# Performance work log

Hardware: AMD Instinct MI355X
Metric: run time of the kernel (lower is better)

The kernel has to match this reference:

```python
import jax, jax.numpy as jnp
import numpy as np

NEG_SLOPE = 0.05

def leaky(x):
    return jnp.where(x >= 0, x, NEG_SLOPE * x)

def segment_softmax(e, seg, num_segments):
    m = jax.ops.segment_max(e, seg, num_segments=num_segments)
    ex = jnp.exp(e - m[seg])
    s = jax.ops.segment_sum(ex, seg, num_segments=num_segments)
    return ex / s[seg]

def scatter_mean(vals, seg, num_segments):
    tot = jax.ops.segment_sum(vals, seg, num_segments=num_segments)
    cnt = jax.ops.segment_sum(jnp.ones((vals.shape[0],), vals.dtype), seg, num_segments=num_segments)
    return tot / jnp.maximum(cnt, 1.0)[:, None]

def setup_inputs() -> dict:
    key = jax.random.key(0)
    ks = jax.random.split(key, 7)
    N, E, Fn, Fe, D = 50000, 800000, 128, 64, 64
    return {
        "x": jax.random.normal(ks[0], (N, Fn), jnp.float32),
        "edge_attr": jax.random.normal(ks[1], (E, Fe), jnp.float32),
        "edge_index": jax.random.randint(ks[2], (2, E), 0, N, jnp.int64),
        "W_node": jax.random.normal(ks[3], (D, Fn), jnp.float32) * 0.05,
        "W_edge": jax.random.normal(ks[4], (D, Fe), jnp.float32) * 0.05,
        "a_node": jax.random.normal(ks[5], (2 * D,), jnp.float32) * 0.05,
        "a_edge": jax.random.normal(ks[6], (2 * D,), jnp.float32) * 0.05,
    }

def reference(x, edge_attr, edge_index, W_node, W_edge, a_node, a_edge):
    N = x.shape[0]
    E = edge_index.shape[1]
    D = W_node.shape[0]
    h = x @ W_node.T           # [N, D]
    g = edge_attr @ W_edge.T   # [E, D]

    # ----- node->node branch (with self loops) -----
    loops = jnp.arange(N, dtype=edge_index.dtype)
    i_idx = jnp.concatenate([edge_index[0], loops])  # targets [E+N]
    j_idx = jnp.concatenate([edge_index[1], loops])  # sources [E+N]
    # attention score a^T [h_i || h_j] split into halves (no concat materialized)
    hi = h @ a_node[:D]   # [N]
    hj = h @ a_node[D:]   # [N]
    e_n = leaky(hi[i_idx] + hj[j_idx])               # [E+N]
    alpha_n = segment_softmax(e_n, i_idx, N)
    x_from_nodes = scatter_mean(alpha_n[:, None] * h[j_idx], i_idx, N)  # [N, D]

    # ----- edge->node branch (each edge attends from both endpoints) -----
    i_idx_e = jnp.concatenate([edge_index[0], edge_index[1]])           # [2E]
    g2 = jnp.concatenate([g, g], axis=0)                                # g[k_idx_e], [2E, D]
    he = h @ a_edge[:D]   # [N]
    ge = g @ a_edge[D:]   # [E]
    ge2 = jnp.concatenate([ge, ge])
    e_e = leaky(he[i_idx_e] + ge2)                                      # [2E]
    alpha_e = segment_softmax(e_e, i_idx_e, N)
    x_from_edges = scatter_mean(alpha_e[:, None] * g2, i_idx_e, N)      # [N, D]

    return jnp.concatenate([leaky(x_from_nodes), leaky(x_from_edges)], axis=-1)  # [N, 2D]
```

## Files before the change

kernel.cpp:

```cpp
#include <hip/hip_runtime.h>
#include <math.h>

#define NEG_SLOPE 0.05f

__device__ __forceinline__ float leaky(float x){ return x >= 0.f ? x : NEG_SLOPE * x; }

__device__ __forceinline__ unsigned short f2bf(float f){
    unsigned u = __float_as_uint(f);
    unsigned r = u + 0x7FFFu + ((u >> 16) & 1u);
    return (unsigned short)(r >> 16);
}
__device__ __forceinline__ float bf2f(unsigned short us){
    return __uint_as_float((unsigned)us << 16);
}

__global__ __launch_bounds__(256) void k_init(int* deg_n, int* deg_o, int* ctr,
        float* __restrict__ vv, const float* __restrict__ We, const float* __restrict__ a_edge, int N){
    int t = blockIdx.x * blockDim.x + threadIdx.x;
    if (t == 0){ ctr[0] = 0; ctr[1] = 0; }
    if (t < 64){
        float s = 0.f;
        for (int d = 0; d < 64; d++) s = fmaf(We[d * 64 + t], a_edge[64 + d], s);
        vv[t] = s;
    }
    int stride = gridDim.x * blockDim.x;
    for (int i = t; i < N; i += stride){ deg_n[i] = 0; deg_o[i] = 0; }
}

__global__ __launch_bounds__(256) void k_gemm_h(const float* __restrict__ A, const float* __restrict__ B,
        const float* __restrict__ a_node, const float* __restrict__ a_edge,
        float* __restrict__ C, unsigned short* __restrict__ Cb,
        float* __restrict__ hi, float* __restrict__ hj, float* __restrict__ he, int M){
    const int K = 128;
    __shared__ float As[K][68];
    __shared__ float Bs[K][68];
    const int m0 = blockIdx.x * 64;
    const int t = threadIdx.x;
    for (int i = t; i < 16 * K; i += 256){
        int d = i & 63, kq = i >> 6;
        float4 b = *(const float4*)&B[(size_t)d * K + kq * 4];
        Bs[kq*4+0][d] = b.x; Bs[kq*4+1][d] = b.y; Bs[kq*4+2][d] = b.z; Bs[kq*4+3][d] = b.w;
    }
    for (int i = t; i < 16 * K; i += 256){
        int r = i & 63, kq = i >> 6;
        int m = m0 + r;
        float4 a = make_float4(0.f, 0.f, 0.f, 0.f);
        if (m < M) a = *(const float4*)&A[(size_t)m * K + kq * 4];
        As[kq*4+0][r] = a.x; As[kq*4+1][r] = a.y; As[kq*4+2][r] = a.z; As[kq*4+3][r] = a.w;
    }
    __syncthreads();
    const int tx = t & 15, ty = t >> 4;
    float acc[4][4] = {};
    #pragma unroll 4
    for (int k = 0; k < K; k++){
        float4 a4 = *(const float4*)&As[k][ty * 4];
        float4 b4 = *(const float4*)&Bs[k][tx * 4];
        float av[4] = {a4.x, a4.y, a4.z, a4.w};
        float bv[4] = {b4.x, b4.y, b4.z, b4.w};
        #pragma unroll
        for (int r = 0; r < 4; r++)
            #pragma unroll
            for (int c = 0; c < 4; c++)
                acc[r][c] = fmaf(av[r], bv[c], acc[r][c]);
    }
    #pragma unroll
    for (int r = 0; r < 4; r++){
        int m = m0 + ty * 4 + r;
        if (m < M){
            float4 o = make_float4(acc[r][0], acc[r][1], acc[r][2], acc[r][3]);
            *(float4*)&C[(size_t)m * 64 + tx * 4] = o;
            uint2 u;
            u.x = (unsigned)f2bf(o.x) | ((unsigned)f2bf(o.y) << 16);
            u.y = (unsigned)f2bf(o.z) | ((unsigned)f2bf(o.w) << 16);
            *(uint2*)&Cb[(size_t)m * 64 + tx * 4] = u;
        }
    }
    float4 an1 = *(const float4*)&a_node[tx * 4];
    float4 an2 = *(const float4*)&a_node[64 + tx * 4];
    float4 ae1 = *(const float4*)&a_edge[tx * 4];
    float p1[4], p2[4], p3[4];
    #pragma unroll
    for (int r = 0; r < 4; r++){
        p1[r] = acc[r][0]*an1.x + acc[r][1]*an1.y + acc[r][2]*an1.z + acc[r][3]*an1.w;
        p2[r] = acc[r][0]*an2.x + acc[r][1]*an2.y + acc[r][2]*an2.z + acc[r][3]*an2.w;
        p3[r] = acc[r][0]*ae1.x + acc[r][1]*ae1.y + acc[r][2]*ae1.z + acc[r][3]*ae1.w;
    }
    #pragma unroll
    for (int m = 1; m < 16; m <<= 1){
        #pragma unroll
        for (int r = 0; r < 4; r++){
            p1[r] += __shfl_xor(p1[r], m);
            p2[r] += __shfl_xor(p2[r], m);
            p3[r] += __shfl_xor(p3[r], m);
        }
    }
    if (tx == 0){
        #pragma unroll
        for (int r = 0; r < 4; r++){
            int m = m0 + ty * 4 + r;
            if (m < M){ hi[m] = p1[r]; hj[m] = p2[r]; he[m] = p3[r]; }
        }
    }
}

__global__ __launch_bounds__(256) void k_ge2(const float* __restrict__ ea, const int* __restrict__ idx,
        const float* __restrict__ vv, float* __restrict__ ge, unsigned short* __restrict__ eab,
        int* __restrict__ deg_n, int* __restrict__ deg_o, int E){
    int l = threadIdx.x & 63;
    int gw = (blockIdx.x * 256 + threadIdx.x) >> 6;
    int nw = (gridDim.x * 256) >> 6;
    int seg = l & 15, rl = l >> 4;
    float4 v4 = *(const float4*)&vv[seg * 4];
    for (int r0 = gw * 4; r0 < E; r0 += nw * 4){
        int row = r0 + rl;
        if (row < E){
            float4 a = *(const float4*)&ea[(size_t)row * 64 + seg * 4];
            float s = a.x*v4.x + a.y*v4.y + a.z*v4.z + a.w*v4.w;
            uint2 u;
            u.x = (unsigned)f2bf(a.x) | ((unsigned)f2bf(a.y) << 16);
            u.y = (unsigned)f2bf(a.z) | ((unsigned)f2bf(a.w) << 16);
            *(uint2*)&eab[(size_t)row * 64 + seg * 4] = u;
            #pragma unroll
            for (int m = 1; m < 16; m <<= 1) s += __shfl_xor(s, m);
            if (seg == 0){
                ge[row] = s;
                int i0 = idx[row], i1 = idx[E + row];
                atomicAdd(&deg_n[i0], 1);
                atomicAdd(&deg_o[i1], 1);
            }
        }
    }
}

__global__ __launch_bounds__(256) void k_off(const int* __restrict__ deg_n, const int* __restrict__ deg_o,
        int* __restrict__ deg_e,
        int* __restrict__ off_n, int* __restrict__ cur_n,
        int* __restrict__ off_e, int* __restrict__ cur_e,
        int* __restrict__ ctr, int N){
    int i = blockIdx.x * 256 + threadIdx.x;
    int lane = threadIdx.x & 63;
    int dn = 0, de = 0;
    if (i < N){
        dn = deg_n[i];
        de = dn + deg_o[i];
    }
    int pn = dn, pe = de;
    #pragma unroll
    for (int d = 1; d < 64; d <<= 1){
        int on = __shfl_up(pn, d), oe = __shfl_up(pe, d);
        if (lane >= d){ pn += on; pe += oe; }
    }
    int base_n = 0, base_e = 0;
    if (lane == 63){
        base_n = atomicAdd(&ctr[0], pn);
        base_e = atomicAdd(&ctr[1], pe);
    }
    base_n = __shfl(base_n, 63);
    base_e = __shfl(base_e, 63);
    if (i < N){
        int on = base_n + pn - dn;
        int oe = base_e + pe - de;
        off_n[i] = on; cur_n[i] = on;
        off_e[i] = oe; cur_e[i] = oe;
        deg_e[i] = de;
    }
}

__global__ __launch_bounds__(256) void k_fill(const int* __restrict__ idx,
        const float* __restrict__ hj, const float* __restrict__ ge,
        int* __restrict__ cur_n, int* __restrict__ cur_e,
        int2* __restrict__ adj_n, int2* __restrict__ adj_e, int E, int N){
    int g = blockIdx.x & 7;
    int lo = (int)(((long long)g * N) >> 3), hi = (int)(((long long)(g + 1) * N) >> 3);
    int nblk = gridDim.x >> 3;
    int start = ((blockIdx.x >> 3) * 256) + threadIdx.x;
    int stride = nblk * 256;
    for (int k = start; k < E; k += stride){
        int i0 = idx[k], i1 = idx[E + k];
        bool t0 = (i0 >= lo && i0 < hi), t1 = (i1 >= lo && i1 < hi);
        if (t0 | t1){
            int gb = __float_as_int(ge[k]);
            if (t0){
                adj_n[atomicAdd(&cur_n[i0], 1)] = make_int2(i1, __float_as_int(hj[i1]));
                adj_e[atomicAdd(&cur_e[i0], 1)] = make_int2(k, gb);
            }
            if (t1) adj_e[atomicAdd(&cur_e[i1], 1)] = make_int2(k, gb);
        }
    }
}

__global__ __launch_bounds__(256) void k_out(const float* __restrict__ h,
        const unsigned short* __restrict__ hb, const unsigned short* __restrict__ eab,
        const float* __restrict__ hi, const float* __restrict__ hj, const float* __restrict__ he,
        const float* __restrict__ We,
        const int* __restrict__ off_n, const int* __restrict__ deg_n, const int2* __restrict__ adj_n,
        const int* __restrict__ off_e, const int* __restrict__ deg_e, const int2* __restrict__ adj_e,
        float* __restrict__ out, int N, int nb_node){
    __shared__ float WeT[64][65];
    __shared__ float valS[4][64];
    int lane = threadIdx.x & 63;
    int w = threadIdx.x >> 6;

    if (blockIdx.x < nb_node){
        int i = (blockIdx.x * 256 + (int)threadIdx.x) >> 6;
        if (i >= N) return;
        float hi_i = hi[i];
        float wself = __expf(leaky(hi_i + hj[i]));
        float s = wself;
        float acc = wself * h[(size_t)i * 64 + lane];
        int cnt = deg_n[i];
        int p = off_n[i], e = p + cnt;
        for (; p + 4 <= e; p += 4){
            int2 r0 = adj_n[p], r1 = adj_n[p+1], r2 = adj_n[p+2], r3 = adj_n[p+3];
            float v0 = bf2f(hb[(size_t)r0.x * 64 + lane]);
            float v1 = bf2f(hb[(size_t)r1.x * 64 + lane]);
            float v2 = bf2f(hb[(size_t)r2.x * 64 + lane]);
            float v3 = bf2f(hb[(size_t)r3.x * 64 + lane]);
            float w0 = __expf(leaky(hi_i + __int_as_float(r0.y)));
            float w1 = __expf(leaky(hi_i + __int_as_float(r1.y)));
            float w2 = __expf(leaky(hi_i + __int_as_float(r2.y)));
            float w3 = __expf(leaky(hi_i + __int_as_float(r3.y)));
            acc = fmaf(w0, v0, acc); acc = fmaf(w1, v1, acc);
            acc = fmaf(w2, v2, acc); acc = fmaf(w3, v3, acc);
            s += (w0 + w1) + (w2 + w3);
        }
        for (; p < e; p++){
            int2 r = adj_n[p];
            float v = bf2f(hb[(size_t)r.x * 64 + lane]);
            float wgt = __expf(leaky(hi_i + __int_as_float(r.y)));
            acc = fmaf(wgt, v, acc); s += wgt;
        }
        out[(size_t)i * 128 + lane] = leaky(acc / s / (float)(cnt + 1));
    } else {
        for (int t2 = threadIdx.x; t2 < 1024; t2 += 256){
            int d = t2 >> 4, c0 = (t2 & 15) * 4;
            float4 v = *(const float4*)&We[d * 64 + c0];
            WeT[c0+0][d] = v.x; WeT[c0+1][d] = v.y; WeT[c0+2][d] = v.z; WeT[c0+3][d] = v.w;
        }
        int i = ((blockIdx.x - nb_node) * 256 + (int)threadIdx.x) >> 6;
        float val = 0.f;
        int iok = (i < N);
        if (iok){
            float he_i = he[i];
            float s = 0.f, acc = 0.f;
            int cnt = deg_e[i];
            int p = off_e[i], e = p + cnt;
            for (; p + 4 <= e; p += 4){
                int2 r0 = adj_e[p], r1 = adj_e[p+1], r2 = adj_e[p+2], r3 = adj_e[p+3];
                float v0 = bf2f(eab[(size_t)r0.x * 64 + lane]);
                float v1 = bf2f(eab[(size_t)r1.x * 64 + lane]);
                float v2 = bf2f(eab[(size_t)r2.x * 64 + lane]);
                float v3 = bf2f(eab[(size_t)r3.x * 64 + lane]);
                float w0 = __expf(leaky(he_i + __int_as_float(r0.y)));
                float w1 = __expf(leaky(he_i + __int_as_float(r1.y)));
                float w2 = __expf(leaky(he_i + __int_as_float(r2.y)));
                float w3 = __expf(leaky(he_i + __int_as_float(r3.y)));
                acc = fmaf(w0, v0, acc); acc = fmaf(w1, v1, acc);
                acc = fmaf(w2, v2, acc); acc = fmaf(w3, v3, acc);
                s += (w0 + w1) + (w2 + w3);
            }
            for (; p < e; p++){
                int2 r = adj_e[p];
                float v = bf2f(eab[(size_t)r.x * 64 + lane]);
                float wgt = __expf(leaky(he_i + __int_as_float(r.y)));
                acc = fmaf(wgt, v, acc); s += wgt;
            }
            val = (cnt > 0) ? (acc / s / (float)cnt) : 0.f;
        }
        __syncthreads();
        valS[w][lane] = val;
        __syncthreads();
        if (iok){
            float acc2 = 0.f;
            #pragma unroll
            for (int c4 = 0; c4 < 16; c4++){
                float4 vb = *(const float4*)&valS[w][c4 * 4];
                acc2 = fmaf(vb.x, WeT[c4*4+0][lane], acc2);
                acc2 = fmaf(vb.y, WeT[c4*4+1][lane], acc2);
                acc2 = fmaf(vb.z, WeT[c4*4+2][lane], acc2);
                acc2 = fmaf(vb.w, WeT[c4*4+3][lane], acc2);
            }
            out[(size_t)i * 128 + 64 + lane] = leaky(acc2);
        }
    }
}

extern "C" void kernel_launch(void* const* d_in, const int* in_sizes, int n_in,
                              void* d_out, int out_size, void* d_ws, size_t ws_size,
                              hipStream_t stream){
    const float* x      = (const float*)d_in[0];
    const float* ea     = (const float*)d_in[1];
    const int*   idx    = (const int*)  d_in[2];
    const float* Wn     = (const float*)d_in[3];
    const float* We     = (const float*)d_in[4];
    const float* a_node = (const float*)d_in[5];
    const float* a_edge = (const float*)d_in[6];
    float* out = (float*)d_out;

    const int N = in_sizes[0] / 128;
    const int E = in_sizes[1] / 64;

    float* p = (float*)d_ws;
    float* h      = p; p += (size_t)N * 64;
    float* hi     = p; p += N;
    float* hj     = p; p += N;
    float* he     = p; p += N;
    float* ge     = p; p += E;
    float* vv     = p; p += 64;
    unsigned short* hb  = (unsigned short*)p; p += (size_t)N * 32;
    unsigned short* eab = (unsigned short*)p; p += (size_t)E * 32;
    int* deg_n = (int*)p; p += N;
    int* deg_o = (int*)p; p += N;
    int* deg_e = (int*)p; p += N;
    int* off_n = (int*)p; p += N;
    int* off_e = (int*)p; p += N;
    int* cur_n = (int*)p; p += N;
    int* cur_e = (int*)p; p += N;
    int* ctr   = (int*)p; p += 4;
    int2* adj_n = (int2*)p; p += (size_t)2 * E;
    int2* adj_e = (int2*)p; p += (size_t)4 * E;

    const int nb = (N + 3) / 4;

    k_init<<<256, 256, 0, stream>>>(deg_n, deg_o, ctr, vv, We, a_edge, N);
    k_gemm_h<<<(N + 63) / 64, 256, 0, stream>>>(x, Wn, a_node, a_edge, h, hb, hi, hj, he, N);
    k_ge2<<<2048, 256, 0, stream>>>(ea, idx, vv, ge, eab, deg_n, deg_o, E);
    k_off<<<(N + 255) / 256, 256, 0, stream>>>(deg_n, deg_o, deg_e, off_n, cur_n, off_e, cur_e, ctr, N);
    k_fill<<<1024, 256, 0, stream>>>(idx, hj, ge, cur_n, cur_e, adj_n, adj_e, E, N);
    k_out<<<2 * nb, 256, 0, stream>>>(h, hb, eab, hi, hj, he, We,
                                      off_n, deg_n, adj_n, off_e, deg_e, adj_e, out, N, nb);
}
```

Before: 611.8 us.

## Vectorize gather rows per quarter-wave and make CSR slices contiguous per fill group

The aggregation kernels now have each 16-lane quarter-wave process a different neighbor, loading 4 bf16 values per lane, so one wave handles 4 neighbors at a time. Partial sums are combined with cross-lane shuffles at the end. The offset computation is split into two passes that compute per-slice totals, so each of the 8 node slices used by the fill kernel gets a contiguous, 64-aligned region of the adjacency arrays. This is meant to improve memory-level parallelism in the gather and locality in the fill scatter, at the cost of an extra kernel launch and more shuffle work.

```diff
diff --git a/kernel.cpp b/kernel.cpp
--- a/kernel.cpp
+++ b/kernel.cpp
@@ -14,10 +14,21 @@
     return __uint_as_float((unsigned)us << 16);
 }
 
-__global__ __launch_bounds__(256) void k_init(int* deg_n, int* deg_o, int* ctr,
+__device__ __forceinline__ int slice_lo(int g, int N){
+    long long v = ((((long long)g * N) >> 3) + 63LL) & ~63LL;
+    return (int)(v > (long long)N ? (long long)N : v);
+}
+__device__ __forceinline__ int slice_of_wave(int w0, int N){
+    int g = 0;
+    #pragma unroll
+    for (int q = 1; q < 8; q++) if (w0 >= slice_lo(q, N)) g = q;
+    return g;
+}
+
+__global__ __launch_bounds__(256) void k_init(int* deg_n, int* deg_o, int* sctr,
         float* __restrict__ vv, const float* __restrict__ We, const float* __restrict__ a_edge, int N){
     int t = blockIdx.x * blockDim.x + threadIdx.x;
-    if (t == 0){ ctr[0] = 0; ctr[1] = 0; }
+    if (t < 32) sctr[t] = 0;
     if (t < 64){
         float s = 0.f;
         for (int d = 0; d < 64; d++) s = fmaf(We[d * 64 + t], a_edge[64 + d], s);
@@ -132,28 +143,48 @@
     }
 }
 
-__global__ __launch_bounds__(256) void k_off(const int* __restrict__ deg_n, const int* __restrict__ deg_o,
+__global__ __launch_bounds__(256) void k_off_a(const int* __restrict__ deg_n, const int* __restrict__ deg_o,
+        int* __restrict__ sctr, int N){
+    int i = blockIdx.x * 256 + threadIdx.x;
+    int lane = threadIdx.x & 63;
+    int dn = 0, de = 0;
+    if (i < N){ dn = deg_n[i]; de = dn + deg_o[i]; }
+    int pn = dn, pe = de;
+    #pragma unroll
+    for (int d = 1; d < 64; d <<= 1){ pn += __shfl_xor(pn, d); pe += __shfl_xor(pe, d); }
+    if (lane == 0){
+        int w0 = i;
+        if (w0 < N){
+            int g = slice_of_wave(w0, N);
+            atomicAdd(&sctr[g], pn);
+            atomicAdd(&sctr[8 + g], pe);
+        }
+    }
+}
+
+__global__ __launch_bounds__(256) void k_off_b(const int* __restrict__ deg_n, const int* __restrict__ deg_o,
         int* __restrict__ deg_e,
         int* __restrict__ off_n, int* __restrict__ cur_n,
         int* __restrict__ off_e, int* __restrict__ cur_e,
-        int* __restrict__ ctr, int N){
+        int* __restrict__ sctr, int N){
     int i = blockIdx.x * 256 + threadIdx.x;
     int lane = threadIdx.x & 63;
     int dn = 0, de = 0;
-    if (i < N){
-        dn = deg_n[i];
-        de = dn + deg_o[i];
-    }
+    if (i < N){ dn = deg_n[i]; de = dn + deg_o[i]; }
     int pn = dn, pe = de;
     #pragma unroll
     for (int d = 1; d < 64; d <<= 1){
         int on = __shfl_up(pn, d), oe = __shfl_up(pe, d);
         if (lane >= d){ pn += on; pe += oe; }
     }
+    int w0 = i - lane;
     int base_n = 0, base_e = 0;
-    if (lane == 63){
-        base_n = atomicAdd(&ctr[0], pn);
-        base_e = atomicAdd(&ctr[1], pe);
+    if (lane == 63 && w0 < N){
+        int g = slice_of_wave(w0, N);
+        int bn = 0, be = 0;
+        for (int q = 0; q < g; q++){ bn += sctr[q]; be += sctr[8 + q]; }
+        base_n = bn + atomicAdd(&sctr[16 + g], pn);
+        base_e = be + atomicAdd(&sctr[24 + g], pe);
     }
     base_n = __shfl(base_n, 63);
     base_e = __shfl(base_e, 63);
@@ -171,7 +202,7 @@
         int* __restrict__ cur_n, int* __restrict__ cur_e,
         int2* __restrict__ adj_n, int2* __restrict__ adj_e, int E, int N){
     int g = blockIdx.x & 7;
-    int lo = (int)(((long long)g * N) >> 3), hi = (int)(((long long)(g + 1) * N) >> 3);
+    int lo = slice_lo(g, N), hi = slice_lo(g + 1, N);
     int nblk = gridDim.x >> 3;
     int start = ((blockIdx.x >> 3) * 256) + threadIdx.x;
     int stride = nblk * 256;
@@ -198,39 +229,74 @@
         float* __restrict__ out, int N, int nb_node){
     __shared__ float WeT[64][65];
     __shared__ float valS[4][64];
-    int lane = threadIdx.x & 63;
-    int w = threadIdx.x >> 6;
+    const int lane = threadIdx.x & 63;
+    const int w = threadIdx.x >> 6;
+    const int rl = lane >> 4, seg = lane & 15;
 
     if (blockIdx.x < nb_node){
         int i = (blockIdx.x * 256 + (int)threadIdx.x) >> 6;
         if (i >= N) return;
         float hi_i = hi[i];
-        float wself = __expf(leaky(hi_i + hj[i]));
-        float s = wself;
-        float acc = wself * h[(size_t)i * 64 + lane];
         int cnt = deg_n[i];
-        int p = off_n[i], e = p + cnt;
-        for (; p + 4 <= e; p += 4){
-            int2 r0 = adj_n[p], r1 = adj_n[p+1], r2 = adj_n[p+2], r3 = adj_n[p+3];
-            float v0 = bf2f(hb[(size_t)r0.x * 64 + lane]);
-            float v1 = bf2f(hb[(size_t)r1.x * 64 + lane]);
-            float v2 = bf2f(hb[(size_t)r2.x * 64 + lane]);
-            float v3 = bf2f(hb[(size_t)r3.x * 64 + lane]);
-            float w0 = __expf(leaky(hi_i + __int_as_float(r0.y)));
-            float w1 = __expf(leaky(hi_i + __int_as_float(r1.y)));
-            float w2 = __expf(leaky(hi_i + __int_as_float(r2.y)));
-            float w3 = __expf(leaky(hi_i + __int_as_float(r3.y)));
-            acc = fmaf(w0, v0, acc); acc = fmaf(w1, v1, acc);
-            acc = fmaf(w2, v2, acc); acc = fmaf(w3, v3, acc);
-            s += (w0 + w1) + (w2 + w3);
-        }
-        for (; p < e; p++){
-            int2 r = adj_n[p];
-            float v = bf2f(hb[(size_t)r.x * 64 + lane]);
-            float wgt = __expf(leaky(hi_i + __int_as_float(r.y)));
-            acc = fmaf(wgt, v, acc); s += wgt;
-        }
-        out[(size_t)i * 128 + lane] = leaky(acc / s / (float)(cnt + 1));
+        int p = off_n[i];
+        int e = p + cnt;
+        float a0 = 0.f, a1 = 0.f, a2 = 0.f, a3 = 0.f, sp = 0.f;
+        for (; p + 8 <= e; p += 8){
+            int2 ra = adj_n[p + rl];
+            int2 rb = adj_n[p + 4 + rl];
+            uint2 ua = *(const uint2*)&hb[(size_t)ra.x * 64 + seg * 4];
+            uint2 ub = *(const uint2*)&hb[(size_t)rb.x * 64 + seg * 4];
+            float wa = __expf(leaky(hi_i + __int_as_float(ra.y)));
+            float wb = __expf(leaky(hi_i + __int_as_float(rb.y)));
+            a0 = fmaf(wa, bf2f((unsigned short)ua.x), a0);
+            a1 = fmaf(wa, bf2f((unsigned short)(ua.x >> 16)), a1);
+            a2 = fmaf(wa, bf2f((unsigned short)ua.y), a2);
+            a3 = fmaf(wa, bf2f((unsigned short)(ua.y >> 16)), a3);
+            a0 = fmaf(wb, bf2f((unsigned short)ub.x), a0);
+            a1 = fmaf(wb, bf2f((unsigned short)(ub.x >> 16)), a1);
+            a2 = fmaf(wb, bf2f((unsigned short)ub.y), a2);
+            a3 = fmaf(wb, bf2f((unsigned short)(ub.y >> 16)), a3);
+            sp += wa + wb;
+        }
+        if (p + 4 <= e){
+            int2 ra = adj_n[p + rl];
+            uint2 ua = *(const uint2*)&hb[(size_t)ra.x * 64 + seg * 4];
+            float wa = __expf(leaky(hi_i + __int_as_float(ra.y)));
+            a0 = fmaf(wa, bf2f((unsigned short)ua.x), a0);
+            a1 = fmaf(wa, bf2f((unsigned short)(ua.x >> 16)), a1);
+            a2 = fmaf(wa, bf2f((unsigned short)ua.y), a2);
+            a3 = fmaf(wa, bf2f((unsigned short)(ua.y >> 16)), a3);
+            sp += wa;
+            p += 4;
+        }
+        int rem = e - p;
+        if (rl < rem){
+            int2 ra = adj_n[p + rl];
+            uint2 ua = *(const uint2*)&hb[(size_t)ra.x * 64 + seg * 4];
+            float wa = __expf(leaky(hi_i + __int_as_float(ra.y)));
+            a0 = fmaf(wa, bf2f((unsigned short)ua.x), a0);
+            a1 = fmaf(wa, bf2f((unsigned short)(ua.x >> 16)), a1);
+            a2 = fmaf(wa, bf2f((unsigned short)ua.y), a2);
+            a3 = fmaf(wa, bf2f((unsigned short)(ua.y >> 16)), a3);
+            sp += wa;
+        }
+        a0 += __shfl_xor(a0, 16); a0 += __shfl_xor(a0, 32);
+        a1 += __shfl_xor(a1, 16); a1 += __shfl_xor(a1, 32);
+        a2 += __shfl_xor(a2, 16); a2 += __shfl_xor(a2, 32);
+        a3 += __shfl_xor(a3, 16); a3 += __shfl_xor(a3, 32);
+        sp += __shfl_xor(sp, 16); sp += __shfl_xor(sp, 32);
+        if (rl == 0){
+            float4 h4 = *(const float4*)&h[(size_t)i * 64 + seg * 4];
+            float wself = __expf(leaky(hi_i + hj[i]));
+            float s = sp + wself;
+            float inv = 1.f / (s * (float)(cnt + 1));
+            float4 o;
+            o.x = leaky(fmaf(wself, h4.x, a0) * inv);
+            o.y = leaky(fmaf(wself, h4.y, a1) * inv);
+            o.z = leaky(fmaf(wself, h4.z, a2) * inv);
+            o.w = leaky(fmaf(wself, h4.w, a3) * inv);
+            *(float4*)&out[(size_t)i * 128 + seg * 4] = o;
+        }
     } else {
         for (int t2 = threadIdx.x; t2 < 1024; t2 += 256){
             int d = t2 >> 4, c0 = (t2 & 15) * 4;
@@ -238,37 +304,65 @@
             WeT[c0+0][d] = v.x; WeT[c0+1][d] = v.y; WeT[c0+2][d] = v.z; WeT[c0+3][d] = v.w;
         }
         int i = ((blockIdx.x - nb_node) * 256 + (int)threadIdx.x) >> 6;
-        float val = 0.f;
-        int iok = (i < N);
+        const int iok = (i < N);
+        float v0 = 0.f, v1 = 0.f, v2 = 0.f, v3 = 0.f;
         if (iok){
             float he_i = he[i];
-            float s = 0.f, acc = 0.f;
             int cnt = deg_e[i];
-            int p = off_e[i], e = p + cnt;
-            for (; p + 4 <= e; p += 4){
-                int2 r0 = adj_e[p], r1 = adj_e[p+1], r2 = adj_e[p+2], r3 = adj_e[p+3];
-                float v0 = bf2f(eab[(size_t)r0.x * 64 + lane]);
-                float v1 = bf2f(eab[(size_t)r1.x * 64 + lane]);
-                float v2 = bf2f(eab[(size_t)r2.x * 64 + lane]);
-                float v3 = bf2f(eab[(size_t)r3.x * 64 + lane]);
-                float w0 = __expf(leaky(he_i + __int_as_float(r0.y)));
-                float w1 = __expf(leaky(he_i + __int_as_float(r1.y)));
-                float w2 = __expf(leaky(he_i + __int_as_float(r2.y)));
-                float w3 = __expf(leaky(he_i + __int_as_float(r3.y)));
-                acc = fmaf(w0, v0, acc); acc = fmaf(w1, v1, acc);
-                acc = fmaf(w2, v2, acc); acc = fmaf(w3, v3, acc);
-                s += (w0 + w1) + (w2 + w3);
-            }
-            for (; p < e; p++){
-                int2 r = adj_e[p];
-                float v = bf2f(eab[(size_t)r.x * 64 + lane]);
-                float wgt = __expf(leaky(he_i + __int_as_float(r.y)));
-                acc = fmaf(wgt, v, acc); s += wgt;
-            }
-            val = (cnt > 0) ? (acc / s / (float)cnt) : 0.f;
+            int p = off_e[i];
+            int e = p + cnt;
+            float a0 = 0.f, a1 = 0.f, a2 = 0.f, a3 = 0.f, sp = 0.f;
+            for (; p + 8 <= e; p += 8){
+                int2 ra = adj_e[p + rl];
+                int2 rb = adj_e[p + 4 + rl];
+                uint2 ua = *(const uint2*)&eab[(size_t)ra.x * 64 + seg * 4];
+                uint2 ub = *(const uint2*)&eab[(size_t)rb.x * 64 + seg * 4];
+                float wa = __expf(leaky(he_i + __int_as_float(ra.y)));
+                float wb = __expf(leaky(he_i + __int_as_float(rb.y)));
+                a0 = fmaf(wa, bf2f((unsigned short)ua.x), a0);
+                a1 = fmaf(wa, bf2f((unsigned short)(ua.x >> 16)), a1);
+                a2 = fmaf(wa, bf2f((unsigned short)ua.y), a2);
+                a3 = fmaf(wa, bf2f((unsigned short)(ua.y >> 16)), a3);
+                a0 = fmaf(wb, bf2f((unsigned short)ub.x), a0);
+                a1 = fmaf(wb, bf2f((unsigned short)(ub.x >> 16)), a1);
+                a2 = fmaf(wb, bf2f((unsigned short)ub.y), a2);
+                a3 = fmaf(wb, bf2f((unsigned short)(ub.y >> 16)), a3);
+                sp += wa + wb;
+            }
+            if (p + 4 <= e){
+                int2 ra = adj_e[p + rl];
+                uint2 ua = *(const uint2*)&eab[(size_t)ra.x * 64 + seg * 4];
+                float wa = __expf(leaky(he_i + __int_as_float(ra.y)));
+                a0 = fmaf(wa, bf2f((unsigned short)ua.x), a0);
+                a1 = fmaf(wa, bf2f((unsigned short)(ua.x >> 16)), a1);
+                a2 = fmaf(wa, bf2f((unsigned short)ua.y), a2);
+                a3 = fmaf(wa, bf2f((unsigned short)(ua.y >> 16)), a3);
+                sp += wa;
+                p += 4;
+            }
+            int rem = e - p;
+            if (rl < rem){
+                int2 ra = adj_e[p + rl];
+                uint2 ua = *(const uint2*)&eab[(size_t)ra.x * 64 + seg * 4];
+                float wa = __expf(leaky(he_i + __int_as_float(ra.y)));
+                a0 = fmaf(wa, bf2f((unsigned short)ua.x), a0);
+                a1 = fmaf(wa, bf2f((unsigned short)(ua.x >> 16)), a1);
+                a2 = fmaf(wa, bf2f((unsigned short)ua.y), a2);
+                a3 = fmaf(wa, bf2f((unsigned short)(ua.y >> 16)), a3);
+                sp += wa;
+            }
+            a0 += __shfl_xor(a0, 16); a0 += __shfl_xor(a0, 32);
+            a1 += __shfl_xor(a1, 16); a1 += __shfl_xor(a1, 32);
+            a2 += __shfl_xor(a2, 16); a2 += __shfl_xor(a2, 32);
+            a3 += __shfl_xor(a3, 16); a3 += __shfl_xor(a3, 32);
+            sp += __shfl_xor(sp, 16); sp += __shfl_xor(sp, 32);
+            if (cnt > 0){
+                float inv = 1.f / (sp * (float)cnt);
+                v0 = a0 * inv; v1 = a1 * inv; v2 = a2 * inv; v3 = a3 * inv;
+            }
         }
         __syncthreads();
-        valS[w][lane] = val;
+        if (rl == 0) *(float4*)&valS[w][seg * 4] = make_float4(v0, v1, v2, v3);
         __syncthreads();
         if (iok){
             float acc2 = 0.f;
@@ -316,16 +410,17 @@
     int* off_e = (int*)p; p += N;
     int* cur_n = (int*)p; p += N;
     int* cur_e = (int*)p; p += N;
-    int* ctr   = (int*)p; p += 4;
+    int* sctr  = (int*)p; p += 32;
     int2* adj_n = (int2*)p; p += (size_t)2 * E;
     int2* adj_e = (int2*)p; p += (size_t)4 * E;
 
     const int nb = (N + 3) / 4;
 
-    k_init<<<256, 256, 0, stream>>>(deg_n, deg_o, ctr, vv, We, a_edge, N);
+    k_init<<<256, 256, 0, stream>>>(deg_n, deg_o, sctr, vv, We, a_edge, N);
     k_gemm_h<<<(N + 63) / 64, 256, 0, stream>>>(x, Wn, a_node, a_edge, h, hb, hi, hj, he, N);
     k_ge2<<<2048, 256, 0, stream>>>(ea, idx, vv, ge, eab, deg_n, deg_o, E);
-    k_off<<<(N + 255) / 256, 256, 0, stream>>>(deg_n, deg_o, deg_e, off_n, cur_n, off_e, cur_e, ctr, N);
+    k_off_a<<<(N + 255) / 256, 256, 0, stream>>>(deg_n, deg_o, sctr, N);
+    k_off_b<<<(N + 255) / 256, 256, 0, stream>>>(deg_n, deg_o, deg_e, off_n, cur_n, off_e, cur_e, sctr, N);
     k_fill<<<1024, 256, 0, stream>>>(idx, hj, ge, cur_n, cur_e, adj_n, adj_e, E, N);
     k_out<<<2 * nb, 256, 0, stream>>>(h, hb, eab, hi, hj, he, We,
                                       off_n, deg_n, adj_n, off_e, deg_e, adj_e, out, N, nb);
```

Measured after the change: 612.8 us. Within noise of the previous version (+0.2%).

## Scatter edge features into CSR order and fuse node and edge aggregation

Applied to the files above, without the earlier changes.

Replaces the index-based adjacency lists with a CSR-ordered copy of the bf16 edge features plus a 16-byte record per slot. Each edge slot carries its score, and slots from the target side also carry the source node index and its hj score. The node branch and the edge branch are now aggregated in one pass per node, so edge features are read contiguously instead of gathered. Degree counting and position filling are partitioned into slices so atomics stay local, and slice-wise prefix sums keep offsets grouped. The cost is that each bf16 edge row is written twice, plus extra kernels and extra record traffic.

```diff
diff --git a/kernel.cpp b/kernel.cpp
--- a/kernel.cpp
+++ b/kernel.cpp
@@ -14,10 +14,21 @@
     return __uint_as_float((unsigned)us << 16);
 }
 
-__global__ __launch_bounds__(256) void k_init(int* deg_n, int* deg_o, int* ctr,
+__device__ __forceinline__ int slice_lo(int g, int N){
+    long long v = ((((long long)g * N) >> 3) + 63LL) & ~63LL;
+    return (int)(v > (long long)N ? (long long)N : v);
+}
+__device__ __forceinline__ int slice_of_wave(int w0, int N){
+    int g = 0;
+    #pragma unroll
+    for (int q = 1; q < 8; q++) if (w0 >= slice_lo(q, N)) g = q;
+    return g;
+}
+
+__global__ __launch_bounds__(256) void k_init(int* deg_n, int* deg_o, int* sctr,
         float* __restrict__ vv, const float* __restrict__ We, const float* __restrict__ a_edge, int N){
     int t = blockIdx.x * blockDim.x + threadIdx.x;
-    if (t == 0){ ctr[0] = 0; ctr[1] = 0; }
+    if (t < 16) sctr[t] = 0;
     if (t < 64){
         float s = 0.f;
         for (int d = 0; d < 64; d++) s = fmaf(We[d * 64 + t], a_edge[64 + d], s);
@@ -103,185 +114,226 @@
     }
 }
 
-__global__ __launch_bounds__(256) void k_ge2(const float* __restrict__ ea, const int* __restrict__ idx,
-        const float* __restrict__ vv, float* __restrict__ ge, unsigned short* __restrict__ eab,
-        int* __restrict__ deg_n, int* __restrict__ deg_o, int E){
+__global__ __launch_bounds__(256) void k_count(const int* __restrict__ idx,
+        int* __restrict__ deg_n, int* __restrict__ deg_o, int E, int N){
+    int g = blockIdx.x & 7;
+    int lo = slice_lo(g, N), hi = slice_lo(g + 1, N);
+    int nblk = gridDim.x >> 3;
+    int start = ((blockIdx.x >> 3) * 256) + threadIdx.x;
+    int stride = nblk * 256;
+    for (int k = start; k < E; k += stride){
+        int i0 = idx[k], i1 = idx[E + k];
+        if (i0 >= lo && i0 < hi) atomicAdd(&deg_n[i0], 1);
+        if (i1 >= lo && i1 < hi) atomicAdd(&deg_o[i1], 1);
+    }
+}
+
+__global__ __launch_bounds__(256) void k_off_a(const int* __restrict__ deg_n, const int* __restrict__ deg_o,
+        int* __restrict__ sctr, int N){
+    int i = blockIdx.x * 256 + threadIdx.x;
+    int lane = threadIdx.x & 63;
+    int de = 0;
+    if (i < N) de = deg_n[i] + deg_o[i];
+    int pe = de;
+    #pragma unroll
+    for (int d = 1; d < 64; d <<= 1) pe += __shfl_xor(pe, d);
+    if (lane == 0 && i < N){
+        int g = slice_of_wave(i, N);
+        atomicAdd(&sctr[g], pe);
+    }
+}
+
+__global__ __launch_bounds__(256) void k_off_b(const int* __restrict__ deg_n, const int* __restrict__ deg_o,
+        int* __restrict__ deg_e, int* __restrict__ off_e, int* __restrict__ cur_e,
+        int* __restrict__ sctr, int N){
+    int i = blockIdx.x * 256 + threadIdx.x;
+    int lane = threadIdx.x & 63;
+    int de = 0;
+    if (i < N) de = deg_n[i] + deg_o[i];
+    int pe = de;
+    #pragma unroll
+    for (int d = 1; d < 64; d <<= 1){
+        int oe = __shfl_up(pe, d);
+        if (lane >= d) pe += oe;
+    }
+    int w0 = i - lane;
+    int base_e = 0;
+    if (lane == 63 && w0 < N){
+        int g = slice_of_wave(w0, N);
+        int be = 0;
+        for (int q = 0; q < g; q++) be += sctr[q];
+        base_e = be + atomicAdd(&sctr[8 + g], pe);
+    }
+    base_e = __shfl(base_e, 63);
+    if (i < N){
+        int oe = base_e + pe - de;
+        off_e[i] = oe; cur_e[i] = oe;
+        deg_e[i] = de;
+    }
+}
+
+__global__ __launch_bounds__(256) void k_fillpos(const int* __restrict__ idx,
+        int* __restrict__ cur_e, int* __restrict__ pos0, int* __restrict__ pos1, int E, int N){
+    int g = blockIdx.x & 7;
+    int lo = slice_lo(g, N), hi = slice_lo(g + 1, N);
+    int nblk = gridDim.x >> 3;
+    int start = ((blockIdx.x >> 3) * 256) + threadIdx.x;
+    int stride = nblk * 256;
+    for (int k = start; k < E; k += stride){
+        int i0 = idx[k], i1 = idx[E + k];
+        if (i0 >= lo && i0 < hi) pos0[k] = atomicAdd(&cur_e[i0], 1);
+        if (i1 >= lo && i1 < hi) pos1[k] = atomicAdd(&cur_e[i1], 1);
+    }
+}
+
+__global__ __launch_bounds__(256) void k_ge3(const float* __restrict__ ea, const int* __restrict__ idx,
+        const int* __restrict__ pos0, const int* __restrict__ pos1,
+        const float* __restrict__ vv, const float* __restrict__ hj,
+        unsigned short* __restrict__ eseq, int4* __restrict__ rec, int E){
     int l = threadIdx.x & 63;
     int gw = (blockIdx.x * 256 + threadIdx.x) >> 6;
     int nw = (gridDim.x * 256) >> 6;
     int seg = l & 15, rl = l >> 4;
+    int leader = rl << 4;
     float4 v4 = *(const float4*)&vv[seg * 4];
     for (int r0 = gw * 4; r0 < E; r0 += nw * 4){
         int row = r0 + rl;
         if (row < E){
             float4 a = *(const float4*)&ea[(size_t)row * 64 + seg * 4];
             float s = a.x*v4.x + a.y*v4.y + a.z*v4.z + a.w*v4.w;
+            #pragma unroll
+            for (int m = 1; m < 16; m <<= 1) s += __shfl_xor(s, m);
             uint2 u;
             u.x = (unsigned)f2bf(a.x) | ((unsigned)f2bf(a.y) << 16);
             u.y = (unsigned)f2bf(a.z) | ((unsigned)f2bf(a.w) << 16);
-            *(uint2*)&eab[(size_t)row * 64 + seg * 4] = u;
-            #pragma unroll
-            for (int m = 1; m < 16; m <<= 1) s += __shfl_xor(s, m);
+            int p0 = 0, p1 = 0;
+            if (seg == 0){ p0 = pos0[row]; p1 = pos1[row]; }
+            p0 = __shfl(p0, leader);
+            p1 = __shfl(p1, leader);
+            *(uint2*)&eseq[(size_t)p0 * 64 + seg * 4] = u;
+            *(uint2*)&eseq[(size_t)p1 * 64 + seg * 4] = u;
             if (seg == 0){
-                ge[row] = s;
                 int i0 = idx[row], i1 = idx[E + row];
-                atomicAdd(&deg_n[i0], 1);
-                atomicAdd(&deg_o[i1], 1);
+                rec[p0] = make_int4((int)((unsigned)i1 | 0x80000000u), __float_as_int(hj[i1]), __float_as_int(s), 0);
+                rec[p1] = make_int4(i0, 0, __float_as_int(s), 0);
             }
         }
     }
 }
 
-__global__ __launch_bounds__(256) void k_off(const int* __restrict__ deg_n, const int* __restrict__ deg_o,
-        int* __restrict__ deg_e,
-        int* __restrict__ off_n, int* __restrict__ cur_n,
-        int* __restrict__ off_e, int* __restrict__ cur_e,
-        int* __restrict__ ctr, int N){
-    int i = blockIdx.x * 256 + threadIdx.x;
-    int lane = threadIdx.x & 63;
-    int dn = 0, de = 0;
-    if (i < N){
-        dn = deg_n[i];
-        de = dn + deg_o[i];
-    }
-    int pn = dn, pe = de;
-    #pragma unroll
-    for (int d = 1; d < 64; d <<= 1){
-        int on = __shfl_up(pn, d), oe = __shfl_up(pe, d);
-        if (lane >= d){ pn += on; pe += oe; }
-    }
-    int base_n = 0, base_e = 0;
-    if (lane == 63){
-        base_n = atomicAdd(&ctr[0], pn);
-        base_e = atomicAdd(&ctr[1], pe);
-    }
-    base_n = __shfl(base_n, 63);
-    base_e = __shfl(base_e, 63);
-    if (i < N){
-        int on = base_n + pn - dn;
-        int oe = base_e + pe - de;
-        off_n[i] = on; cur_n[i] = on;
-        off_e[i] = oe; cur_e[i] = oe;
-        deg_e[i] = de;
-    }
-}
-
-__global__ __launch_bounds__(256) void k_fill(const int* __restrict__ idx,
-        const float* __restrict__ hj, const float* __restrict__ ge,
-        int* __restrict__ cur_n, int* __restrict__ cur_e,
-        int2* __restrict__ adj_n, int2* __restrict__ adj_e, int E, int N){
-    int g = blockIdx.x & 7;
-    int lo = (int)(((long long)g * N) >> 3), hi = (int)(((long long)(g + 1) * N) >> 3);
-    int nblk = gridDim.x >> 3;
-    int start = ((blockIdx.x >> 3) * 256) + threadIdx.x;
-    int stride = nblk * 256;
-    for (int k = start; k < E; k += stride){
-        int i0 = idx[k], i1 = idx[E + k];
-        bool t0 = (i0 >= lo && i0 < hi), t1 = (i1 >= lo && i1 < hi);
-        if (t0 | t1){
-            int gb = __float_as_int(ge[k]);
-            if (t0){
-                adj_n[atomicAdd(&cur_n[i0], 1)] = make_int2(i1, __float_as_int(hj[i1]));
-                adj_e[atomicAdd(&cur_e[i0], 1)] = make_int2(k, gb);
-            }
-            if (t1) adj_e[atomicAdd(&cur_e[i1], 1)] = make_int2(k, gb);
-        }
-    }
-}
-
 __global__ __launch_bounds__(256) void k_out(const float* __restrict__ h,
-        const unsigned short* __restrict__ hb, const unsigned short* __restrict__ eab,
+        const unsigned short* __restrict__ hb, const unsigned short* __restrict__ eseq,
+        const int4* __restrict__ rec,
         const float* __restrict__ hi, const float* __restrict__ hj, const float* __restrict__ he,
         const float* __restrict__ We,
-        const int* __restrict__ off_n, const int* __restrict__ deg_n, const int2* __restrict__ adj_n,
-        const int* __restrict__ off_e, const int* __restrict__ deg_e, const int2* __restrict__ adj_e,
-        float* __restrict__ out, int N, int nb_node){
+        const int* __restrict__ off_e, const int* __restrict__ deg_e, const int* __restrict__ deg_n,
+        float* __restrict__ out, int N){
     __shared__ float WeT[64][65];
     __shared__ float valS[4][64];
-    int lane = threadIdx.x & 63;
-    int w = threadIdx.x >> 6;
-
-    if (blockIdx.x < nb_node){
-        int i = (blockIdx.x * 256 + (int)threadIdx.x) >> 6;
-        if (i >= N) return;
-        float hi_i = hi[i];
+    const int lane = threadIdx.x & 63;
+    const int w = threadIdx.x >> 6;
+    const int rl = lane >> 4, seg = lane & 15;
+
+    for (int t2 = threadIdx.x; t2 < 1024; t2 += 256){
+        int d = t2 >> 4, c0 = (t2 & 15) * 4;
+        float4 v = *(const float4*)&We[d * 64 + c0];
+        WeT[c0+0][d] = v.x; WeT[c0+1][d] = v.y; WeT[c0+2][d] = v.z; WeT[c0+3][d] = v.w;
+    }
+
+    int i = (blockIdx.x * 256 + (int)threadIdx.x) >> 6;
+    const bool iok = (i < N);
+    float an0=0.f, an1=0.f, an2=0.f, an3=0.f, sn=0.f;
+    float ae0=0.f, ae1=0.f, ae2=0.f, ae3=0.f, se=0.f;
+    float hi_i = 0.f, he_i = 0.f;
+    int cnt = 0, cntn = 0;
+    if (iok){
+        hi_i = hi[i]; he_i = he[i];
+        cnt = deg_e[i]; cntn = deg_n[i];
+        int p = off_e[i], e = p + cnt;
+        for (; p + 4 <= e; p += 4){
+            int4 r = rec[p + rl];
+            uint2 ue = *(const uint2*)&eseq[(size_t)(p + rl) * 64 + seg * 4];
+            float we_ = __expf(leaky(he_i + __int_as_float(r.z)));
+            ae0 = fmaf(we_, bf2f((unsigned short)ue.x), ae0);
+            ae1 = fmaf(we_, bf2f((unsigned short)(ue.x >> 16)), ae1);
+            ae2 = fmaf(we_, bf2f((unsigned short)ue.y), ae2);
+            ae3 = fmaf(we_, bf2f((unsigned short)(ue.y >> 16)), ae3);
+            se += we_;
+            if (r.x < 0){
+                int j = r.x & 0x7fffffff;
+                float wn_ = __expf(leaky(hi_i + __int_as_float(r.y)));
+                uint2 un = *(const uint2*)&hb[(size_t)j * 64 + seg * 4];
+                an0 = fmaf(wn_, bf2f((unsigned short)un.x), an0);
+                an1 = fmaf(wn_, bf2f((unsigned short)(un.x >> 16)), an1);
+                an2 = fmaf(wn_, bf2f((unsigned short)un.y), an2);
+                an3 = fmaf(wn_, bf2f((unsigned short)(un.y >> 16)), an3);
+                sn += wn_;
+            }
+        }
+        int rem = e - p;
+        if (rl < rem){
+            int4 r = rec[p + rl];
+            uint2 ue = *(const uint2*)&eseq[(size_t)(p + rl) * 64 + seg * 4];
+            float we_ = __expf(leaky(he_i + __int_as_float(r.z)));
+            ae0 = fmaf(we_, bf2f((unsigned short)ue.x), ae0);
+            ae1 = fmaf(we_, bf2f((unsigned short)(ue.x >> 16)), ae1);
+            ae2 = fmaf(we_, bf2f((unsigned short)ue.y), ae2);
+            ae3 = fmaf(we_, bf2f((unsigned short)(ue.y >> 16)), ae3);
+            se += we_;
+            if (r.x < 0){
+                int j = r.x & 0x7fffffff;
+                float wn_ = __expf(leaky(hi_i + __int_as_float(r.y)));
+                uint2 un = *(const uint2*)&hb[(size_t)j * 64 + seg * 4];
+                an0 = fmaf(wn_, bf2f((unsigned short)un.x), an0);
+                an1 = fmaf(wn_, bf2f((unsigned short)(un.x >> 16)), an1);
+                an2 = fmaf(wn_, bf2f((unsigned short)un.y), an2);
+                an3 = fmaf(wn_, bf2f((unsigned short)(un.y >> 16)), an3);
+                sn += wn_;
+            }
+        }
+    }
+    an0 += __shfl_xor(an0, 16); an0 += __shfl_xor(an0, 32);
+    an1 += __shfl_xor(an1, 16); an1 += __shfl_xor(an1, 32);
+    an2 += __shfl_xor(an2, 16); an2 += __shfl_xor(an2, 32);
+    an3 += __shfl_xor(an3, 16); an3 += __shfl_xor(an3, 32);
+    sn  += __shfl_xor(sn, 16);  sn  += __shfl_xor(sn, 32);
+    ae0 += __shfl_xor(ae0, 16); ae0 += __shfl_xor(ae0, 32);
+    ae1 += __shfl_xor(ae1, 16); ae1 += __shfl_xor(ae1, 32);
+    ae2 += __shfl_xor(ae2, 16); ae2 += __shfl_xor(ae2, 32);
+    ae3 += __shfl_xor(ae3, 16); ae3 += __shfl_xor(ae3, 32);
+    se  += __shfl_xor(se, 16);  se  += __shfl_xor(se, 32);
+
+    if (iok && rl == 0){
+        float4 h4 = *(const float4*)&h[(size_t)i * 64 + seg * 4];
         float wself = __expf(leaky(hi_i + hj[i]));
-        float s = wself;
-        float acc = wself * h[(size_t)i * 64 + lane];
-        int cnt = deg_n[i];
-        int p = off_n[i], e = p + cnt;
-        for (; p + 4 <= e; p += 4){
-            int2 r0 = adj_n[p], r1 = adj_n[p+1], r2 = adj_n[p+2], r3 = adj_n[p+3];
-            float v0 = bf2f(hb[(size_t)r0.x * 64 + lane]);
-            float v1 = bf2f(hb[(size_t)r1.x * 64 + lane]);
-            float v2 = bf2f(hb[(size_t)r2.x * 64 + lane]);
-            float v3 = bf2f(hb[(size_t)r3.x * 64 + lane]);
-            float w0 = __expf(leaky(hi_i + __int_as_float(r0.y)));
-            float w1 = __expf(leaky(hi_i + __int_as_float(r1.y)));
-            float w2 = __expf(leaky(hi_i + __int_as_float(r2.y)));
-            float w3 = __expf(leaky(hi_i + __int_as_float(r3.y)));
-            acc = fmaf(w0, v0, acc); acc = fmaf(w1, v1, acc);
-            acc = fmaf(w2, v2, acc); acc = fmaf(w3, v3, acc);
-            s += (w0 + w1) + (w2 + w3);
-        }
-        for (; p < e; p++){
-            int2 r = adj_n[p];
-            float v = bf2f(hb[(size_t)r.x * 64 + lane]);
-            float wgt = __expf(leaky(hi_i + __int_as_float(r.y)));
-            acc = fmaf(wgt, v, acc); s += wgt;
-        }
-        out[(size_t)i * 128 + lane] = leaky(acc / s / (float)(cnt + 1));
-    } else {
-        for (int t2 = threadIdx.x; t2 < 1024; t2 += 256){
-            int d = t2 >> 4, c0 = (t2 & 15) * 4;
-            float4 v = *(const float4*)&We[d * 64 + c0];
-            WeT[c0+0][d] = v.x; WeT[c0+1][d] = v.y; WeT[c0+2][d] = v.z; WeT[c0+3][d] = v.w;
-        }
-        int i = ((blockIdx.x - nb_node) * 256 + (int)threadIdx.x) >> 6;
-        float val = 0.f;
-        int iok = (i < N);
-        if (iok){
-            float he_i = he[i];
-            float s = 0.f, acc = 0.f;
-            int cnt = deg_e[i];
-            int p = off_e[i], e = p + cnt;
-            for (; p + 4 <= e; p += 4){
-                int2 r0 = adj_e[p], r1 = adj_e[p+1], r2 = adj_e[p+2], r3 = adj_e[p+3];
-                float v0 = bf2f(eab[(size_t)r0.x * 64 + lane]);
-                float v1 = bf2f(eab[(size_t)r1.x * 64 + lane]);
-                float v2 = bf2f(eab[(size_t)r2.x * 64 + lane]);
-                float v3 = bf2f(eab[(size_t)r3.x * 64 + lane]);
-                float w0 = __expf(leaky(he_i + __int_as_float(r0.y)));
-                float w1 = __expf(leaky(he_i + __int_as_float(r1.y)));
-                float w2 = __expf(leaky(he_i + __int_as_float(r2.y)));
-                float w3 = __expf(leaky(he_i + __int_as_float(r3.y)));
-                acc = fmaf(w0, v0, acc); acc = fmaf(w1, v1, acc);
-                acc = fmaf(w2, v2, acc); acc = fmaf(w3, v3, acc);
-                s += (w0 + w1) + (w2 + w3);
-            }
-            for (; p < e; p++){
-                int2 r = adj_e[p];
-                float v = bf2f(eab[(size_t)r.x * 64 + lane]);
-                float wgt = __expf(leaky(he_i + __int_as_float(r.y)));
-                acc = fmaf(wgt, v, acc); s += wgt;
-            }
-            val = (cnt > 0) ? (acc / s / (float)cnt) : 0.f;
-        }
-        __syncthreads();
-        valS[w][lane] = val;
-        __syncthreads();
-        if (iok){
-            float acc2 = 0.f;
-            #pragma unroll
-            for (int c4 = 0; c4 < 16; c4++){
-                float4 vb = *(const float4*)&valS[w][c4 * 4];
-                acc2 = fmaf(vb.x, WeT[c4*4+0][lane], acc2);
-                acc2 = fmaf(vb.y, WeT[c4*4+1][lane], acc2);
-                acc2 = fmaf(vb.z, WeT[c4*4+2][lane], acc2);
-                acc2 = fmaf(vb.w, WeT[c4*4+3][lane], acc2);
-            }
-            out[(size_t)i * 128 + 64 + lane] = leaky(acc2);
-        }
+        float s = sn + wself;
+        float inv = 1.f / (s * (float)(cntn + 1));
+        float4 o;
+        o.x = leaky(fmaf(wself, h4.x, an0) * inv);
+        o.y = leaky(fmaf(wself, h4.y, an1) * inv);
+        o.z = leaky(fmaf(wself, h4.z, an2) * inv);
+        o.w = leaky(fmaf(wself, h4.w, an3) * inv);
+        *(float4*)&out[(size_t)i * 128 + seg * 4] = o;
+    }
+    float v0 = 0.f, v1 = 0.f, v2 = 0.f, v3 = 0.f;
+    if (iok && cnt > 0){
+        float inv = 1.f / (se * (float)cnt);
+        v0 = ae0 * inv; v1 = ae1 * inv; v2 = ae2 * inv; v3 = ae3 * inv;
+    }
+    __syncthreads();
+    if (rl == 0) *(float4*)&valS[w][seg * 4] = make_float4(v0, v1, v2, v3);
+    __syncthreads();
+    if (iok){
+        float acc2 = 0.f;
+        #pragma unroll
+        for (int c4 = 0; c4 < 16; c4++){
+            float4 vb = *(const float4*)&valS[w][c4 * 4];
+            acc2 = fmaf(vb.x, WeT[c4*4+0][lane], acc2);
+            acc2 = fmaf(vb.y, WeT[c4*4+1][lane], acc2);
+            acc2 = fmaf(vb.z, WeT[c4*4+2][lane], acc2);
+            acc2 = fmaf(vb.w, WeT[c4*4+3][lane], acc2);
+        }
+        out[(size_t)i * 128 + 64 + lane] = leaky(acc2);
     }
 }
 
@@ -305,28 +357,27 @@
     float* hi     = p; p += N;
     float* hj     = p; p += N;
     float* he     = p; p += N;
-    float* ge     = p; p += E;
     float* vv     = p; p += 64;
-    unsigned short* hb  = (unsigned short*)p; p += (size_t)N * 32;
-    unsigned short* eab = (unsigned short*)p; p += (size_t)E * 32;
+    unsigned short* hb = (unsigned short*)p; p += (size_t)N * 32;
     int* deg_n = (int*)p; p += N;
     int* deg_o = (int*)p; p += N;
     int* deg_e = (int*)p; p += N;
-    int* off_n = (int*)p; p += N;
     int* off_e = (int*)p; p += N;
-    int* cur_n = (int*)p; p += N;
     int* cur_e = (int*)p; p += N;
-    int* ctr   = (int*)p; p += 4;
-    int2* adj_n = (int2*)p; p += (size_t)2 * E;
-    int2* adj_e = (int2*)p; p += (size_t)4 * E;
-
-    const int nb = (N + 3) / 4;
-
-    k_init<<<256, 256, 0, stream>>>(deg_n, deg_o, ctr, vv, We, a_edge, N);
+    int* pos0  = (int*)p; p += E;
+    int* pos1  = (int*)p; p += E;
+    int* sctr  = (int*)p; p += 16;
+    p = (float*)(((size_t)p + 15) & ~(size_t)15);
+    int4* rec = (int4*)p; p += (size_t)2 * E * 4;
+    unsigned short* eseq = (unsigned short*)p;
+
+    k_init<<<256, 256, 0, stream>>>(deg_n, deg_o, sctr, vv, We, a_edge, N);
     k_gemm_h<<<(N + 63) / 64, 256, 0, stream>>>(x, Wn, a_node, a_edge, h, hb, hi, hj, he, N);
-    k_ge2<<<2048, 256, 0, stream>>>(ea, idx, vv, ge, eab, deg_n, deg_o, E);
-    k_off<<<(N + 255) / 256, 256, 0, stream>>>(deg_n, deg_o, deg_e, off_n, cur_n, off_e, cur_e, ctr, N);
-    k_fill<<<1024, 256, 0, stream>>>(idx, hj, ge, cur_n, cur_e, adj_n, adj_e, E, N);
-    k_out<<<2 * nb, 256, 0, stream>>>(h, hb, eab, hi, hj, he, We,
-                                      off_n, deg_n, adj_n, off_e, deg_e, adj_e, out, N, nb);
-}
+    k_count<<<1024, 256, 0, stream>>>(idx, deg_n, deg_o, E, N);
+    k_off_a<<<(N + 255) / 256, 256, 0, stream>>>(deg_n, deg_o, sctr, N);
+    k_off_b<<<(N + 255) / 256, 256, 0, stream>>>(deg_n, deg_o, deg_e, off_e, cur_e, sctr, N);
+    k_fillpos<<<1024, 256, 0, stream>>>(idx, cur_e, pos0, pos1, E, N);
+    k_ge3<<<2048, 256, 0, stream>>>(ea, idx, pos0, pos1, vv, hj, eseq, rec, E);
+    k_out<<<(N + 3) / 4, 256, 0, stream>>>(h, hb, eseq, rec, hi, hj, he, We,
+                                           off_e, deg_e, deg_n, out, N);
+}
```

After: 716.1 us. 17.0% more time.
